# Optimization experiments

Measured on AMD Instinct MI355X. Metric: run time of the kernel, lower is better.

The kernel has to match this reference:

```python
import jax, jax.numpy as jnp
import numpy as np


def _procrustes_align(X, Y):
    """Batched similarity-transform (scipy-style Procrustes, reflection allowed).
    Aligns Y (pred) to X (target). X, Y: [B, N, 3]. Returns aligned Y: [B, N, 3].
    """
    muX = X.mean(axis=1, keepdims=True)                      # [B,1,3]
    muY = Y.mean(axis=1, keepdims=True)
    X0 = X - muX
    Y0 = Y - muY
    normX = jnp.sqrt((X0 ** 2).sum(axis=(1, 2), keepdims=True))  # [B,1,1]
    normY = jnp.sqrt((Y0 ** 2).sum(axis=(1, 2), keepdims=True))
    X0n = X0 / normX
    Y0n = Y0 / normY
    # 3x3 cross-covariance per batch element
    M = jnp.einsum('bni,bnj->bij', X0n, Y0n)                 # [B,3,3]
    U, s, Vt = jnp.linalg.svd(M)                             # batched tiny SVD
    # Optimal rotation Q = V @ U^T = (U @ Vt)^T  (minimizes ||Y0n @ Q - X0n||)
    Q = jnp.swapaxes(jnp.matmul(U, Vt), -1, -2)              # [B,3,3]
    traceTA = s.sum(-1)[:, None, None]                       # [B,1,1]
    Z = normX * traceTA * jnp.einsum('bni,bij->bnj', Y0n, Q) + muX
    return Z


def setup_inputs() -> dict:
    key = jax.random.key(0)
    k1, k2 = jax.random.split(key)
    B, N = 262144, 21
    pred_kp3d = jax.random.normal(k1, (B, N, 3), dtype=jnp.float32)
    target_kp3d = jax.random.normal(k2, (B, N, 3), dtype=jnp.float32)
    return {"pred_kp3d": pred_kp3d, "target_kp3d": target_kp3d}


def reference(pred_kp3d, target_kp3d):
    pred_aligned = _procrustes_align(target_kp3d, pred_kp3d)
    # mean per-joint Euclidean distance (PA-MPJPE style)
    err = jnp.sqrt(((pred_aligned - target_kp3d) ** 2).sum(-1)).mean()
    return err
```

## Files before the change

### kernel.cpp

```cpp
#include <hip/hip_runtime.h>
#include <math.h>

#define NPTS 21
#define FLB  63
#define BPB  128
#define THREADS 128

__global__ void pa_init(float* out) {
    if (threadIdx.x == 0 && blockIdx.x == 0) out[0] = 0.0f;
}

__global__ __launch_bounds__(THREADS, 2)
void pa_mpjpe(const float* __restrict__ pred,
              const float* __restrict__ targ,
              float* __restrict__ out,
              int B, float inv_total)
{
    __shared__ __align__(16) float sbuf[BPB * FLB];
    __shared__ float swsum[THREADS / 64];

    const int tid  = threadIdx.x;
    const int b0   = blockIdx.x * BPB;
    const int nb   = (B - b0 < BPB) ? (B - b0) : BPB;
    const int nflt = nb * FLB;
    const int nvec = nflt >> 2;

    {
        const float4* g = (const float4*)(pred + (size_t)b0 * FLB);
        float4* s = (float4*)sbuf;
        for (int i = tid; i < nvec; i += THREADS) s[i] = g[i];
        const float* gf = pred + (size_t)b0 * FLB;
        for (int i = (nvec << 2) + tid; i < nflt; i += THREADS) sbuf[i] = gf[i];
    }
    __syncthreads();

    float y[NPTS][3];
    float sy0 = 0.f, sy1 = 0.f, sy2 = 0.f, syy = 0.f;
    const int base = tid * FLB;
    #pragma unroll
    for (int n = 0; n < NPTS; ++n) {
        float a = sbuf[base + 3*n + 0];
        float b = sbuf[base + 3*n + 1];
        float c = sbuf[base + 3*n + 2];
        y[n][0] = a; y[n][1] = b; y[n][2] = c;
        sy0 += a; sy1 += b; sy2 += c;
        syy = fmaf(a, a, fmaf(b, b, fmaf(c, c, syy)));
    }
    __syncthreads();

    {
        const float4* g = (const float4*)(targ + (size_t)b0 * FLB);
        float4* s = (float4*)sbuf;
        for (int i = tid; i < nvec; i += THREADS) s[i] = g[i];
        const float* gf = targ + (size_t)b0 * FLB;
        for (int i = (nvec << 2) + tid; i < nflt; i += THREADS) sbuf[i] = gf[i];
    }
    __syncthreads();

    float sx0 = 0.f, sx1 = 0.f, sx2 = 0.f;
    float m00=0,m01=0,m02=0, m10=0,m11=0,m12=0, m20=0,m21=0,m22=0;
    #pragma unroll
    for (int n = 0; n < NPTS; ++n) {
        float a = sbuf[base + 3*n + 0];
        float b = sbuf[base + 3*n + 1];
        float c = sbuf[base + 3*n + 2];
        sx0 += a; sx1 += b; sx2 += c;
        float u = y[n][0], v = y[n][1], w = y[n][2];
        m00 = fmaf(a,u,m00); m01 = fmaf(a,v,m01); m02 = fmaf(a,w,m02);
        m10 = fmaf(b,u,m10); m11 = fmaf(b,v,m11); m12 = fmaf(b,w,m12);
        m20 = fmaf(c,u,m20); m21 = fmaf(c,v,m21); m22 = fmaf(c,w,m22);
    }

    const float invN = 1.0f / (float)NPTS;
    float mux0 = sx0*invN, mux1 = sx1*invN, mux2 = sx2*invN;
    float muy0 = sy0*invN, muy1 = sy1*invN, muy2 = sy2*invN;
    float ny2  = syy - (sy0*sy0 + sy1*sy1 + sy2*sy2) * invN;
    float c00 = m00 - sx0*sy0*invN, c01 = m01 - sx0*sy1*invN, c02 = m02 - sx0*sy2*invN;
    float c10 = m10 - sx1*sy0*invN, c11 = m11 - sx1*sy1*invN, c12 = m12 - sx1*sy2*invN;
    float c20 = m20 - sx2*sy0*invN, c21 = m21 - sx2*sy1*invN, c22 = m22 - sx2*sy2*invN;

    float q00=c00, q01=c10, q02=c20,
          q10=c01, q11=c11, q12=c21,
          q20=c02, q21=c12, q22=c22;
    #pragma unroll
    for (int it = 0; it < 8; ++it) {
        float C00 = q11*q22 - q12*q21;
        float C01 = q12*q20 - q10*q22;
        float C02 = q10*q21 - q11*q20;
        float C10 = q02*q21 - q01*q22;
        float C11 = q00*q22 - q02*q20;
        float C12 = q01*q20 - q00*q21;
        float C20 = q01*q12 - q02*q11;
        float C21 = q02*q10 - q00*q12;
        float C22 = q00*q11 - q01*q10;
        float det = q00*C00 + q01*C01 + q02*C02;
        float ad  = fmaxf(fabsf(det), 1e-30f);
        float sdet = copysignf(ad, det);
        float g  = __expf(0.333333333f * __logf(ad));
        float ha = 0.5f / g;
        float hb = 0.5f * g / sdet;
        q00 = ha*q00 + hb*C00; q01 = ha*q01 + hb*C01; q02 = ha*q02 + hb*C02;
        q10 = ha*q10 + hb*C10; q11 = ha*q11 + hb*C11; q12 = ha*q12 + hb*C12;
        q20 = ha*q20 + hb*C20; q21 = ha*q21 + hb*C21; q22 = ha*q22 + hb*C22;
    }

    float trP = q00*c00 + q01*c10 + q02*c20
              + q10*c01 + q11*c11 + q12*c21
              + q20*c02 + q21*c12 + q22*c22;
    float k = trP / ny2;
    float r00=k*q00, r01=k*q01, r02=k*q02;
    float r10=k*q10, r11=k*q11, r12=k*q12;
    float r20=k*q20, r21=k*q21, r22=k*q22;

    float errsum = 0.0f;
    #pragma unroll
    for (int n = 0; n < NPTS; ++n) {
        float xa = sbuf[base + 3*n + 0];
        float xb = sbuf[base + 3*n + 1];
        float xc = sbuf[base + 3*n + 2];
        float u = y[n][0] - muy0, v = y[n][1] - muy1, w = y[n][2] - muy2;
        float z0 = fmaf(u, r00, fmaf(v, r10, fmaf(w, r20, mux0))) - xa;
        float z1 = fmaf(u, r01, fmaf(v, r11, fmaf(w, r21, mux1))) - xb;
        float z2 = fmaf(u, r02, fmaf(v, r12, fmaf(w, r22, mux2))) - xc;
        errsum += sqrtf(fmaf(z0, z0, fmaf(z1, z1, z2*z2)));
    }
    if (tid >= nb) errsum = 0.0f;

    #pragma unroll
    for (int off = 32; off > 0; off >>= 1) errsum += __shfl_down(errsum, off, 64);
    if ((tid & 63) == 0) swsum[tid >> 6] = errsum;
    __syncthreads();
    if (tid == 0) {
        float tot = swsum[0];
        #pragma unroll
        for (int wv = 1; wv < THREADS / 64; ++wv) tot += swsum[wv];
        atomicAdd(out, tot * inv_total);
    }
}

extern "C" void kernel_launch(void* const* d_in, const int* in_sizes, int n_in,
                              void* d_out, int out_size, void* d_ws, size_t ws_size,
                              hipStream_t stream)
{
    const float* pred = (const float*)d_in[0];
    const float* targ = (const float*)d_in[1];
    float* out = (float*)d_out;

    int B = in_sizes[0] / FLB;
    float inv_total = 1.0f / ((float)B * (float)NPTS);

    pa_init<<<1, 64, 0, stream>>>(out);
    int grid = (B + BPB - 1) / BPB;
    pa_mpjpe<<<grid, THREADS, 0, stream>>>(pred, targ, out, B, inv_total);
}
```

Baseline: 173.5 us.

## Use direct global-to-LDS async loads and replace atomics with two-pass reduction

Global-to-shared staging now uses the global_load_lds builtin, so the data no longer passes through VGPRs. Each block writes its partial sum to workspace, and a separate single-block kernel does the final reduction, replacing the init kernel and the per-block atomicAdd. The partial-block tail guard is removed, so correctness now assumes B is a multiple of 128, which holds for the test size. The launch_bounds occupancy hint is also relaxed.

New measurement: 149.5 us. 1.16x faster.

```diff
diff --git a/kernel.cpp b/kernel.cpp
--- a/kernel.cpp
+++ b/kernel.cpp
@@ -5,33 +5,40 @@
 #define FLB  63
 #define BPB  128
 #define THREADS 128
+#define NVEC (BPB * FLB / 4)
+#define FULL_ROUNDS (NVEC / THREADS)
+#define TAIL_LANES  (NVEC % THREADS)
 
-__global__ void pa_init(float* out) {
-    if (threadIdx.x == 0 && blockIdx.x == 0) out[0] = 0.0f;
+__device__ __forceinline__ void async_cp16(const float* g, float* l) {
+    __builtin_amdgcn_global_load_lds(
+        (__attribute__((address_space(1))) void*)g,
+        (__attribute__((address_space(3))) void*)l,
+        16, 0, 0);
 }
 
-__global__ __launch_bounds__(THREADS, 2)
+__global__ __launch_bounds__(THREADS)
 void pa_mpjpe(const float* __restrict__ pred,
               const float* __restrict__ targ,
-              float* __restrict__ out,
-              int B, float inv_total)
+              float* __restrict__ ws,
+              int B)
 {
     __shared__ __align__(16) float sbuf[BPB * FLB];
     __shared__ float swsum[THREADS / 64];
 
     const int tid  = threadIdx.x;
+    const int lane_u = tid & ~63;
     const int b0   = blockIdx.x * BPB;
-    const int nb   = (B - b0 < BPB) ? (B - b0) : BPB;
-    const int nflt = nb * FLB;
-    const int nvec = nflt >> 2;
 
     {
-        const float4* g = (const float4*)(pred + (size_t)b0 * FLB);
-        float4* s = (float4*)sbuf;
-        for (int i = tid; i < nvec; i += THREADS) s[i] = g[i];
-        const float* gf = pred + (size_t)b0 * FLB;
-        for (int i = (nvec << 2) + tid; i < nflt; i += THREADS) sbuf[i] = gf[i];
+        const float* gp = pred + (size_t)b0 * FLB;
+        #pragma unroll
+        for (int j = 0; j < FULL_ROUNDS; ++j)
+            async_cp16(gp + 4 * (j * THREADS + tid), sbuf + 4 * (j * THREADS + lane_u));
+        if (tid < TAIL_LANES)
+            async_cp16(gp + 4 * (FULL_ROUNDS * THREADS + tid),
+                       sbuf + 4 * (FULL_ROUNDS * THREADS + lane_u));
     }
+    __builtin_amdgcn_s_waitcnt(0x0F70);
     __syncthreads();
 
     float y[NPTS][3];
@@ -49,12 +56,15 @@
     __syncthreads();
 
     {
-        const float4* g = (const float4*)(targ + (size_t)b0 * FLB);
-        float4* s = (float4*)sbuf;
-        for (int i = tid; i < nvec; i += THREADS) s[i] = g[i];
-        const float* gf = targ + (size_t)b0 * FLB;
-        for (int i = (nvec << 2) + tid; i < nflt; i += THREADS) sbuf[i] = gf[i];
+        const float* gt = targ + (size_t)b0 * FLB;
+        #pragma unroll
+        for (int j = 0; j < FULL_ROUNDS; ++j)
+            async_cp16(gt + 4 * (j * THREADS + tid), sbuf + 4 * (j * THREADS + lane_u));
+        if (tid < TAIL_LANES)
+            async_cp16(gt + 4 * (FULL_ROUNDS * THREADS + tid),
+                       sbuf + 4 * (FULL_ROUNDS * THREADS + lane_u));
     }
+    __builtin_amdgcn_s_waitcnt(0x0F70);
     __syncthreads();
 
     float sx0 = 0.f, sx1 = 0.f, sx2 = 0.f;
@@ -124,18 +134,27 @@
         float z2 = fmaf(u, r02, fmaf(v, r12, fmaf(w, r22, mux2))) - xc;
         errsum += sqrtf(fmaf(z0, z0, fmaf(z1, z1, z2*z2)));
     }
-    if (tid >= nb) errsum = 0.0f;
 
     #pragma unroll
     for (int off = 32; off > 0; off >>= 1) errsum += __shfl_down(errsum, off, 64);
     if ((tid & 63) == 0) swsum[tid >> 6] = errsum;
     __syncthreads();
-    if (tid == 0) {
-        float tot = swsum[0];
-        #pragma unroll
-        for (int wv = 1; wv < THREADS / 64; ++wv) tot += swsum[wv];
-        atomicAdd(out, tot * inv_total);
-    }
+    if (tid == 0) ws[blockIdx.x] = swsum[0] + swsum[1];
+}
+
+__global__ __launch_bounds__(256)
+void pa_reduce(const float* __restrict__ ws, float* __restrict__ out,
+               int nblk, float inv_total)
+{
+    __shared__ float sw[4];
+    float s = 0.0f;
+    for (int i = threadIdx.x; i < nblk; i += 256) s += ws[i];
+    #pragma unroll
+    for (int off = 32; off > 0; off >>= 1) s += __shfl_down(s, off, 64);
+    if ((threadIdx.x & 63) == 0) sw[threadIdx.x >> 6] = s;
+    __syncthreads();
+    if (threadIdx.x == 0)
+        out[0] = (sw[0] + sw[1] + sw[2] + sw[3]) * inv_total;
 }
 
 extern "C" void kernel_launch(void* const* d_in, const int* in_sizes, int n_in,
@@ -145,11 +164,12 @@
     const float* pred = (const float*)d_in[0];
     const float* targ = (const float*)d_in[1];
     float* out = (float*)d_out;
+    float* ws  = (float*)d_ws;
 
     int B = in_sizes[0] / FLB;
+    int grid = (B + BPB - 1) / BPB;
     float inv_total = 1.0f / ((float)B * (float)NPTS);
 
-    pa_init<<<1, 64, 0, stream>>>(out);
-    int grid = (B + BPB - 1) / BPB;
-    pa_mpjpe<<<grid, THREADS, 0, stream>>>(pred, targ, out, B, inv_total);
+    pa_mpjpe<<<grid, THREADS, 0, stream>>>(pred, targ, ws, B);
+    pa_reduce<<<1, 256, 0, stream>>>(ws, out, grid, inv_total);
 }
```
